# Kernel tuning notes

Measured on AMD Instinct MI355X. Metric: run time of the kernel, lower is better.

The kernel has to match this reference:

```python
import jax, jax.numpy as jnp
import numpy as np

B, N, F, H, E = 2, 384, 64, 128, 4
EPS_MEAN = 1e-10


def _lin(x, W, b=None):
    y = x @ W
    return y if b is None else y + b


def setup_inputs() -> dict:
    key = jax.random.key(0)
    ks = jax.random.split(key, 22)
    def rn(k, shape):
        return (jax.random.normal(k, shape, jnp.float32) / np.sqrt(shape[0])).astype(jnp.float32)
    h = jax.random.normal(ks[0], (B, N, F), jnp.float32)
    coord = jax.random.normal(ks[1], (B, N, 3), jnp.float32)
    edge_attr = jax.random.normal(ks[2], (B, N, N, E), jnp.float32)
    node_attr = jax.random.normal(ks[3], (B, N, F), jnp.float32)
    mask = (jax.random.uniform(ks[4], (B, N)) > 0.2).astype(jnp.float32)
    d_in_edge = 2 * F + 1 + E  # source, target, radial, edge_attr
    return dict(
        h=h, coord=coord, edge_attr=edge_attr, node_attr=node_attr, mask=mask,
        We1=rn(ks[5], (d_in_edge, H)), be1=jnp.zeros((H,), jnp.float32),
        We2=rn(ks[6], (H, H)), be2=jnp.zeros((H,), jnp.float32),
        Wa1=rn(ks[7], (H, H)), ba1=jnp.zeros((H,), jnp.float32),
        Wa2=rn(ks[8], (H, 1)), ba2=jnp.zeros((1,), jnp.float32),
        Wn1=rn(ks[9], (H + F + F, H)), bn1=jnp.zeros((H,), jnp.float32),
        Wn2=rn(ks[10], (H, F)), bn2=jnp.zeros((F,), jnp.float32),
        Wc1=rn(ks[11], (H, H)), bc1=jnp.zeros((H,), jnp.float32),
        Wc2=(jax.random.normal(ks[12], (H, 1), jnp.float32) * 0.001),  # xavier gain=0.001, no bias
    )


def reference(h, coord, edge_attr, node_attr, mask,
              We1, be1, We2, be2, Wa1, ba1, Wa2, ba2,
              Wn1, bn1, Wn2, bn2, Wc1, bc1, Wc2):
    # mask inputs
    coord = coord * mask[..., None]
    h = h * mask[..., None]
    mask2d = mask[:, :, None] * mask[:, None, :]  # [B,N,N]

    # coord2radial
    coord_diff = coord[:, :, None, :] - coord[:, None, :, :]      # [B,N,N,3]
    radial = jnp.sum(coord_diff ** 2, axis=-1, keepdims=True)     # [B,N,N,1]
    radial = radial * mask2d[..., None]
    coord_diff = coord_diff * mask2d[..., None]

    # edge model: source[b,i,j]=h[b,j], target[b,i,j]=h[b,i]
    source = jnp.broadcast_to(h[:, None, :, :], (h.shape[0], h.shape[1], h.shape[1], h.shape[2]))
    target = jnp.broadcast_to(h[:, :, None, :], source.shape)
    einp = jnp.concatenate([source, target, radial, edge_attr], axis=-1)  # [B,N,N,2F+1+E]
    m = jnp.tanh(_lin(einp, We1, be1))
    m = jnp.tanh(_lin(m, We2, be2))
    attn = jax.nn.sigmoid(_lin(jnp.tanh(_lin(m, Wa1, ba1)), Wa2, ba2))
    edge_feat = m * attn                                           # [B,N,N,H]

    # coord model (coords_agg='mean')
    embed_edge = _lin(jnp.tanh(_lin(edge_feat, Wc1, bc1)), Wc2)    # [B,N,N,1]
    trans = coord_diff * embed_edge * mask2d[..., None]            # [B,N,N,3]
    denom = jnp.sum(mask2d, axis=2, keepdims=True) + EPS_MEAN      # [B,N,1]
    coord_out = coord + jnp.sum(trans, axis=2) / denom
    coord_out = coord_out * mask[..., None]

    # node model (residual)
    agg = jnp.sum(edge_feat, axis=2)                               # [B,N,H]
    ninp = jnp.concatenate([h, node_attr, agg], axis=-1) * mask[..., None]
    nout = _lin(jnp.tanh(_lin(ninp, Wn1, bn1)), Wn2, bn2)
    h_out = (h + nout) * mask[..., None]

    return h_out, coord_out, edge_feat
```

## Files before the change

### kernel.cpp

```cpp
#include <hip/hip_runtime.h>

#define BB 2
#define NN 384
#define FF 64
#define HH 128
#define EE 4
#define ETILE 64
#define NCHUNK (NN / ETILE)
#define PRE_NB 16
#define NODE_NB 8

using f4 = float4;
typedef __attribute__((ext_vector_type(8))) short          bf16x8;
typedef __attribute__((ext_vector_type(8))) unsigned short u16x8;
typedef __attribute__((ext_vector_type(4))) unsigned short u16x4;
typedef __attribute__((ext_vector_type(4))) unsigned int   u32x4;
typedef __attribute__((ext_vector_type(4))) float          f32x4;

__device__ __forceinline__ float fast_tanh(float x) {
    float e = __expf(2.0f * x);
    return 1.0f - 2.0f / (e + 1.0f);
}
__device__ __forceinline__ float fast_sigmoid(float x) {
    return 1.0f / (1.0f + __expf(-x));
}
__device__ __forceinline__ unsigned short f2bf(float x) {
    unsigned int u = __float_as_uint(x);
    unsigned int r = (u + 0x7fffu + ((u >> 16) & 1u)) >> 16;
    return (unsigned short)r;
}
__device__ __forceinline__ float bf2f(unsigned short h) {
    return __uint_as_float(((unsigned int)h) << 16);
}
__device__ __forceinline__ bf16x8 as_bf16x8(u32x4 v) {
    union { u32x4 u; bf16x8 b; } c; c.u = v; return c.b;
}

__global__ __launch_bounds__(128) void pre_kernel(
    const float* __restrict__ h, const float* __restrict__ mask,
    const float* __restrict__ We1, const float* __restrict__ be1,
    float* __restrict__ Sg, float* __restrict__ Tg)
{
    const int n0 = blockIdx.x * PRE_NB;
    const int t  = threadIdx.x;
    __shared__ float hl[PRE_NB][FF];
    for (int q = t; q < PRE_NB * FF; q += 128) {
        const int n = q >> 6, f = q & 63;
        hl[n][f] = h[(n0 + n) * FF + f] * mask[n0 + n];
    }
    __syncthreads();
    float accS[PRE_NB], accT[PRE_NB];
    const float b1 = be1[t];
#pragma unroll
    for (int n = 0; n < PRE_NB; ++n) { accS[n] = 0.f; accT[n] = b1; }
    for (int f = 0; f < FF; ++f) {
        const float ws = We1[f * HH + t];
        const float wt = We1[(FF + f) * HH + t];
#pragma unroll
        for (int n = 0; n < PRE_NB; ++n) {
            accS[n] = fmaf(hl[n][f], ws, accS[n]);
            accT[n] = fmaf(hl[n][f], wt, accT[n]);
        }
    }
#pragma unroll
    for (int n = 0; n < PRE_NB; ++n) {
        Sg[(n0 + n) * HH + t] = accS[n];
        Tg[(n0 + n) * HH + t] = accT[n];
    }
}

__global__ __launch_bounds__(128) void wconv_kernel(
    const float* __restrict__ W0, const float* __restrict__ W1,
    const float* __restrict__ W2, unsigned short* __restrict__ WT)
{
    const int mat = blockIdx.x >> 7;
    const int o   = blockIdx.x & 127;
    const int k   = threadIdx.x;
    const float* src = (mat == 0) ? W0 : (mat == 1) ? W1 : W2;
    const float w = src[k * HH + o];
    const unsigned short hi = f2bf(w);
    const unsigned short lo = f2bf(w - bf2f(hi));
    WT[(mat * 2 + 0) * 16384 + o * HH + k] = hi;
    WT[(mat * 2 + 1) * 16384 + o * HH + k] = lo;
}

__device__ __forceinline__ void mfma_pass_dual(
    const ushort* __restrict__ A1, const ushort* __restrict__ A2,
    const ushort* __restrict__ WTp, f32x4 acc[4][2],
    const int l15, const int l4, const int c0)
{
    u32x4 Bf[2][4];
#pragma unroll
    for (int ct = 0; ct < 2; ++ct)
#pragma unroll
        for (int kb = 0; kb < 4; ++kb)
            Bf[ct][kb] = *(const u32x4*)&WTp[(c0 + ct * 16 + l15) * HH + kb * 32 + l4 * 8];
#pragma unroll
    for (int rt = 0; rt < 4; ++rt) {
        bf16x8 Af1[4], Af2[4];
#pragma unroll
        for (int kb = 0; kb < 4; ++kb) {
            const int idx = (16 * rt + l15) * HH + (((kb * 4 + l4) ^ l15) * 8);
            Af1[kb] = *(const bf16x8*)&A1[idx];
            Af2[kb] = *(const bf16x8*)&A2[idx];
        }
#pragma unroll
        for (int ct = 0; ct < 2; ++ct)
#pragma unroll
            for (int kb = 0; kb < 4; ++kb)
                acc[rt][ct] = __builtin_amdgcn_mfma_f32_16x16x32_bf16(
                    Af1[kb], as_bf16x8(Bf[ct][kb]), acc[rt][ct], 0, 0, 0);
#pragma unroll
        for (int ct = 0; ct < 2; ++ct)
#pragma unroll
            for (int kb = 0; kb < 4; ++kb)
                acc[rt][ct] = __builtin_amdgcn_mfma_f32_16x16x32_bf16(
                    Af2[kb], as_bf16x8(Bf[ct][kb]), acc[rt][ct], 0, 0, 0);
    }
}

__device__ __forceinline__ void mfma_pass_single(
    const ushort* __restrict__ A1, const ushort* __restrict__ WTp,
    f32x4 acc[4][2], const int l15, const int l4, const int c0)
{
    u32x4 Bf[2][4];
#pragma unroll
    for (int ct = 0; ct < 2; ++ct)
#pragma unroll
        for (int kb = 0; kb < 4; ++kb)
            Bf[ct][kb] = *(const u32x4*)&WTp[(c0 + ct * 16 + l15) * HH + kb * 32 + l4 * 8];
#pragma unroll
    for (int rt = 0; rt < 4; ++rt) {
        bf16x8 Af1[4];
#pragma unroll
        for (int kb = 0; kb < 4; ++kb) {
            const int idx = (16 * rt + l15) * HH + (((kb * 4 + l4) ^ l15) * 8);
            Af1[kb] = *(const bf16x8*)&A1[idx];
        }
#pragma unroll
        for (int ct = 0; ct < 2; ++ct)
#pragma unroll
            for (int kb = 0; kb < 4; ++kb)
                acc[rt][ct] = __builtin_amdgcn_mfma_f32_16x16x32_bf16(
                    Af1[kb], as_bf16x8(Bf[ct][kb]), acc[rt][ct], 0, 0, 0);
    }
}

__global__ __launch_bounds__(256, 4) void edge_kernel(
    const float* __restrict__ coord, const float* __restrict__ edge_attr,
    const float* __restrict__ mask,  const float* __restrict__ We1,
    const float* __restrict__ be2,   const float* __restrict__ ba1,
    const float* __restrict__ Wa2,   const float* __restrict__ ba2,
    const float* __restrict__ bc1,   const float* __restrict__ Wc2,
    const float* __restrict__ Sg,    const float* __restrict__ Tg,
    const unsigned short* __restrict__ WT,
    float* __restrict__ ef_out,
    float* __restrict__ agg_part,
    float* __restrict__ cag_part)
{
    __shared__ ushort Ah[ETILE * HH];
    __shared__ ushort Al[ETILE * HH];
    __shared__ float Tb[HH];
    __shared__ float sd_l[ETILE];
    __shared__ float cd_l[ETILE][3];
    __shared__ float ea_l[ETILE][4];
    __shared__ float attn_l[ETILE];
    __shared__ float embed_l[ETILE];
    __shared__ float part[512];

    const int bid = blockIdx.x;
    const int jc  = bid % NCHUNK;
    const int i   = (bid / NCHUNK) % NN;
    const int b   = bid / (NCHUNK * NN);
    const int j0  = jc * ETILE;
    const int t   = threadIdx.x;
    const int e   = t & 63;
    const int wv  = __builtin_amdgcn_readfirstlane(t >> 6);
    const int l15 = e & 15, l4 = e >> 4;
    const int c0  = wv * 32;

    const unsigned short* We2h = WT;
    const unsigned short* We2l = WT + 16384;
    const unsigned short* Wa1h = WT + 32768;
    const unsigned short* Wa1l = WT + 49152;
    const unsigned short* Wc1h = WT + 65536;

    const float be2a = be2[c0 + l15],      be2b = be2[c0 + 16 + l15];
    const float ba1a = ba1[c0 + l15],      ba1b = ba1[c0 + 16 + l15];
    const float wa2a = Wa2[c0 + l15],      wa2b = Wa2[c0 + 16 + l15];
    const float bc1a = bc1[c0 + l15],      bc1b = bc1[c0 + 16 + l15];
    const float wc2a = Wc2[c0 + l15],      wc2b = Wc2[c0 + 16 + l15];
    const float ba2s = ba2[0];

    if (t < HH) Tb[t] = Tg[(b * NN + i) * HH + t];
    if (t < ETILE) {
        const int j = j0 + t;
        const float mi = mask[b * NN + i], mj = mask[b * NN + j];
        const float m2 = mi * mj;
        const float d0 = coord[(b * NN + i) * 3 + 0] * mi - coord[(b * NN + j) * 3 + 0] * mj;
        const float d1 = coord[(b * NN + i) * 3 + 1] * mi - coord[(b * NN + j) * 3 + 1] * mj;
        const float d2 = coord[(b * NN + i) * 3 + 2] * mi - coord[(b * NN + j) * 3 + 2] * mj;
        sd_l[t] = (d0 * d0 + d1 * d1 + d2 * d2) * m2;
        cd_l[t][0] = d0 * m2; cd_l[t][1] = d1 * m2; cd_l[t][2] = d2 * m2;
        const f4 ea = *(const f4*)&edge_attr[(((size_t)b * NN + i) * NN + j) * EE];
        ea_l[t][0] = ea.x; ea_l[t][1] = ea.y; ea_l[t][2] = ea.z; ea_l[t][3] = ea.w;
    }
    __syncthreads();

    {
        const float rad = sd_l[e];
        const float ea0 = ea_l[e][0], ea1 = ea_l[e][1], ea2 = ea_l[e][2], ea3 = ea_l[e][3];
        const float* Srow = &Sg[((size_t)b * NN + (j0 + e)) * HH];
#pragma unroll
        for (int s = 0; s < 4; ++s) {
            u16x8 hp, lp;
#pragma unroll
            for (int hq = 0; hq < 2; ++hq) {
                const int o = c0 + s * 8 + hq * 4;
                const f4 sv = *(const f4*)&Srow[o];
                const f4 tb = *(const f4*)&Tb[o];
                const f4 wr = *(const f4*)&We1[128 * HH + o];
                const f4 w0 = *(const f4*)&We1[129 * HH + o];
                const f4 w1 = *(const f4*)&We1[130 * HH + o];
                const f4 w2 = *(const f4*)&We1[131 * HH + o];
                const f4 w3 = *(const f4*)&We1[132 * HH + o];
                float pv[4];
                pv[0] = sv.x + tb.x + rad * wr.x + ea0 * w0.x + ea1 * w1.x + ea2 * w2.x + ea3 * w3.x;
                pv[1] = sv.y + tb.y + rad * wr.y + ea0 * w0.y + ea1 * w1.y + ea2 * w2.y + ea3 * w3.y;
                pv[2] = sv.z + tb.z + rad * wr.z + ea0 * w0.z + ea1 * w1.z + ea2 * w2.z + ea3 * w3.z;
                pv[3] = sv.w + tb.w + rad * wr.w + ea0 * w0.w + ea1 * w1.w + ea2 * w2.w + ea3 * w3.w;
#pragma unroll
                for (int q = 0; q < 4; ++q) {
                    const float v = fast_tanh(pv[q]);
                    const unsigned short hv = f2bf(v);
                    hp[hq * 4 + q] = hv;
                    lp[hq * 4 + q] = f2bf(v - bf2f(hv));
                }
            }
            const int phys = (wv * 4 + s) ^ (e & 15);
            *(u16x8*)&Ah[e * HH + phys * 8] = hp;
            *(u16x8*)&Al[e * HH + phys * 8] = lp;
        }
    }
    __syncthreads();

    f32x4 acc[4][2];

#pragma unroll
    for (int rt = 0; rt < 4; ++rt)
#pragma unroll
        for (int ct = 0; ct < 2; ++ct) acc[rt][ct] = (f32x4){0.f, 0.f, 0.f, 0.f};
    mfma_pass_dual(Ah, Al, We2h, acc, l15, l4, c0);
    mfma_pass_single(Ah, We2l, acc, l15, l4, c0);
    __syncthreads();
#pragma unroll
    for (int rt = 0; rt < 4; ++rt)
#pragma unroll
        for (int ct = 0; ct < 2; ++ct)
#pragma unroll
            for (int r = 0; r < 4; ++r) {
                const float v = fast_tanh(acc[rt][ct][r] + (ct ? be2b : be2a));
                const int row = 16 * rt + 4 * l4 + r;
                const int col = c0 + ct * 16 + l15;
                const int idx = row * HH + (((col >> 3) ^ (row & 15)) * 8) + (col & 7);
                const unsigned short hv = f2bf(v);
                Ah[idx] = hv;
                Al[idx] = f2bf(v - bf2f(hv));
            }
    __syncthreads();

#pragma unroll
    for (int rt = 0; rt < 4; ++rt)
#pragma unroll
        for (int ct = 0; ct < 2; ++ct) acc[rt][ct] = (f32x4){0.f, 0.f, 0.f, 0.f};
    mfma_pass_dual(Ah, Al, Wa1h, acc, l15, l4, c0);
    mfma_pass_single(Ah, Wa1l, acc, l15, l4, c0);
#pragma unroll
    for (int rt = 0; rt < 4; ++rt)
#pragma unroll
        for (int r = 0; r < 4; ++r) {
            float s = fast_tanh(acc[rt][0][r] + ba1a) * wa2a +
                      fast_tanh(acc[rt][1][r] + ba1b) * wa2b;
            s += __shfl_xor(s, 1); s += __shfl_xor(s, 2);
            s += __shfl_xor(s, 4); s += __shfl_xor(s, 8);
            if (l15 == 0) part[wv * 64 + 16 * rt + 4 * l4 + r] = s;
        }
    __syncthreads();
    if (t < ETILE)
        attn_l[t] = fast_sigmoid(part[t] + part[64 + t] + part[128 + t] +
                                 part[192 + t] + ba2s);
    __syncthreads();

#pragma unroll
    for (int rt = 0; rt < 4; ++rt)
#pragma unroll
        for (int ct = 0; ct < 2; ++ct) acc[rt][ct] = (f32x4){0.f, 0.f, 0.f, 0.f};
    mfma_pass_single(Ah, Wc1h, acc, l15, l4, c0);
#pragma unroll
    for (int rt = 0; rt < 4; ++rt)
#pragma unroll
        for (int r = 0; r < 4; ++r) {
            const int row = 16 * rt + 4 * l4 + r;
            const float at = attn_l[row];
            float s = fast_tanh(at * acc[rt][0][r] + bc1a) * wc2a +
                      fast_tanh(at * acc[rt][1][r] + bc1b) * wc2b;
            s += __shfl_xor(s, 1); s += __shfl_xor(s, 2);
            s += __shfl_xor(s, 4); s += __shfl_xor(s, 8);
            if (l15 == 0) part[wv * 64 + row] = s;
        }
    __syncthreads();
    if (t < ETILE)
        embed_l[t] = part[t] + part[64 + t] + part[128 + t] + part[192 + t];
    __syncthreads();

    {
        const int erow = t >> 5;
        const int colq = t & 31;
        const int col  = colq * 4;
        const int chunk = col >> 3;
        const int sub   = col & 7;
        float a0 = 0.f, a1 = 0.f, a2 = 0.f, a3 = 0.f;
        float* obase = &ef_out[(((size_t)b * NN + i) * NN + j0) * HH];
#pragma unroll
        for (int it = 0; it < 8; ++it) {
            const int row = it * 8 + erow;
            const float at = attn_l[row];
            const int idx = row * HH + ((chunk ^ (row & 15)) * 8) + sub;
            const u16x4 hv4 = *(const u16x4*)&Ah[idx];
            const u16x4 lv4 = *(const u16x4*)&Al[idx];
            f4 v;
            v.x = (bf2f(hv4[0]) + bf2f(lv4[0])) * at;
            v.y = (bf2f(hv4[1]) + bf2f(lv4[1])) * at;
            v.z = (bf2f(hv4[2]) + bf2f(lv4[2])) * at;
            v.w = (bf2f(hv4[3]) + bf2f(lv4[3])) * at;
            *(f4*)&obase[row * HH + col] = v;
            a0 += v.x; a1 += v.y; a2 += v.z; a3 += v.w;
        }
        a0 += __shfl_xor(a0, 32);
        a1 += __shfl_xor(a1, 32);
        a2 += __shfl_xor(a2, 32);
        a3 += __shfl_xor(a3, 32);
        if (e < 32) {
            part[wv * HH + col + 0] = a0;
            part[wv * HH + col + 1] = a1;
            part[wv * HH + col + 2] = a2;
            part[wv * HH + col + 3] = a3;
        }
    }
    if (t < ETILE) {
        const float em = embed_l[t];
        float tr0 = cd_l[t][0] * em, tr1 = cd_l[t][1] * em, tr2 = cd_l[t][2] * em;
#pragma unroll
        for (int off = 1; off < 64; off <<= 1) {
            tr0 += __shfl_xor(tr0, off);
            tr1 += __shfl_xor(tr1, off);
            tr2 += __shfl_xor(tr2, off);
        }
        if (t == 0) {
            cag_part[(size_t)bid * 3 + 0] = tr0;
            cag_part[(size_t)bid * 3 + 1] = tr1;
            cag_part[(size_t)bid * 3 + 2] = tr2;
        }
    }
    __syncthreads();
    if (t < HH)
        agg_part[(size_t)bid * HH + t] =
            part[t] + part[HH + t] + part[2 * HH + t] + part[3 * HH + t];
}

__global__ __launch_bounds__(256) void node_kernel(
    const float* __restrict__ h, const float* __restrict__ coord,
    const float* __restrict__ node_attr, const float* __restrict__ mask,
    const float* __restrict__ Wn1, const float* __restrict__ bn1,
    const float* __restrict__ Wn2, const float* __restrict__ bn2,
    const float* __restrict__ agg_part, const float* __restrict__ cag_part,
    float* __restrict__ h_out, float* __restrict__ c_out)
{
    const int n0 = blockIdx.x * NODE_NB;
    const int b  = n0 / NN;
    const int t  = threadIdx.x;
    __shared__ float nl[NODE_NB][2 * FF + HH];
    __shared__ float ul[NODE_NB][HH];
    __shared__ float pp[4][NODE_NB][HH];
    __shared__ float msum_s;

    for (int q = t; q < NODE_NB * 256; q += 256) {
        const int n = q >> 8, k = q & 255;
        const int bn = n0 + n;
        const float mi = mask[bn];
        float v;
        if (k < FF)          v = h[bn * FF + k] * mi;
        else if (k < 2 * FF) v = node_attr[bn * FF + (k - FF)] * mi;
        else {
            float a = 0.f;
            const int o = k - 2 * FF;
#pragma unroll
            for (int jc = 0; jc < NCHUNK; ++jc)
                a += agg_part[((size_t)bn * NCHUNK + jc) * HH + o];
            v = a * mi;
        }
        nl[n][k] = v;
    }
    if (t < 64) {
        float s = 0.f;
#pragma unroll
        for (int q = 0; q < 6; ++q) s += mask[b * NN + q * 64 + t];
#pragma unroll
        for (int off = 1; off < 64; off <<= 1) s += __shfl_xor(s, off);
        if (t == 0) msum_s = s;
    }
    __syncthreads();

    {
        const int col = t & 127, kh = t >> 7;
        float acc[NODE_NB];
#pragma unroll
        for (int n = 0; n < NODE_NB; ++n) acc[n] = 0.f;
        for (int k = kh * 128; k < kh * 128 + 128; ++k) {
            const float w = Wn1[k * HH + col];
#pragma unroll
            for (int n = 0; n < NODE_NB; ++n)
                acc[n] = fmaf(nl[n][k], w, acc[n]);
        }
#pragma unroll
        for (int n = 0; n < NODE_NB; ++n) pp[kh][n][col] = acc[n];
    }
    __syncthreads();
#pragma unroll
    for (int r = 0; r < 4; ++r) {
        const int idx = t + 256 * r;
        const int n = idx >> 7, col = idx & 127;
        ul[n][col] = fast_tanh(pp[0][n][col] + pp[1][n][col] + bn1[col]);
    }
    __syncthreads();

    {
        const int col = t & 63, ks = t >> 6;
        float acc[NODE_NB];
#pragma unroll
        for (int n = 0; n < NODE_NB; ++n) acc[n] = 0.f;
        for (int k = ks * 32; k < ks * 32 + 32; ++k) {
            const float w = Wn2[k * FF + col];
#pragma unroll
            for (int n = 0; n < NODE_NB; ++n)
                acc[n] = fmaf(ul[n][k], w, acc[n]);
        }
#pragma unroll
        for (int n = 0; n < NODE_NB; ++n) pp[ks][n][col] = acc[n];
    }
    __syncthreads();
#pragma unroll
    for (int r = 0; r < 2; ++r) {
        const int idx = t + 256 * r;
        const int n = idx >> 6, col = idx & 63;
        const int bn = n0 + n;
        const float mi = mask[bn];
        const float a = pp[0][n][col] + pp[1][n][col] + pp[2][n][col] +
                        pp[3][n][col] + bn2[col];
        h_out[bn * FF + col] = (nl[n][col] + a) * mi;
    }
    if (t < NODE_NB * 3) {
        const int n = t / 3, d = t % 3;
        const int bn = n0 + n;
        const float mi = mask[bn];
        float cag = 0.f;
#pragma unroll
        for (int jc = 0; jc < NCHUNK; ++jc)
            cag += cag_part[((size_t)bn * NCHUNK + jc) * 3 + d];
        const float denom = mi * msum_s + 1e-10f;
        c_out[bn * 3 + d] = (coord[bn * 3 + d] * mi + cag / denom) * mi;
    }
}

extern "C" void kernel_launch(void* const* d_in, const int* in_sizes, int n_in,
                              void* d_out, int out_size, void* d_ws, size_t ws_size,
                              hipStream_t stream)
{
    const float* h         = (const float*)d_in[0];
    const float* coord     = (const float*)d_in[1];
    const float* edge_attr = (const float*)d_in[2];
    const float* node_attr = (const float*)d_in[3];
    const float* mask      = (const float*)d_in[4];
    const float* We1 = (const float*)d_in[5];
    const float* be1 = (const float*)d_in[6];
    const float* We2 = (const float*)d_in[7];
    const float* be2 = (const float*)d_in[8];
    const float* Wa1 = (const float*)d_in[9];
    const float* ba1 = (const float*)d_in[10];
    const float* Wa2 = (const float*)d_in[11];
    const float* ba2 = (const float*)d_in[12];
    const float* Wn1 = (const float*)d_in[13];
    const float* bn1 = (const float*)d_in[14];
    const float* Wn2 = (const float*)d_in[15];
    const float* bn2 = (const float*)d_in[16];
    const float* Wc1 = (const float*)d_in[17];
    const float* bc1 = (const float*)d_in[18];
    const float* Wc2 = (const float*)d_in[19];

    float* out    = (float*)d_out;
    float* h_out  = out;
    float* c_out  = out + (size_t)BB * NN * FF;
    float* ef_out = c_out + (size_t)BB * NN * 3;

    float* ws = (float*)d_ws;
    float* Sg = ws;
    float* Tg = Sg + (size_t)BB * NN * HH;
    float* agg_part = Tg + (size_t)BB * NN * HH;
    float* cag_part = agg_part + (size_t)BB * NN * NCHUNK * HH;
    unsigned short* WT = (unsigned short*)(cag_part + (size_t)BB * NN * NCHUNK * 3);

    pre_kernel<<<BB * NN / PRE_NB, 128, 0, stream>>>(h, mask, We1, be1, Sg, Tg);
    wconv_kernel<<<3 * HH, 128, 0, stream>>>(We2, Wa1, Wc1, WT);
    edge_kernel<<<BB * NN * NCHUNK, 256, 0, stream>>>(
        coord, edge_attr, mask, We1, be2, ba1, Wa2, ba2, bc1, Wc2,
        Sg, Tg, WT, ef_out, agg_part, cag_part);
    node_kernel<<<BB * NN / NODE_NB, 256, 0, stream>>>(
        h, coord, node_attr, mask, Wn1, bn1, Wn2, bn2,
        agg_part, cag_part, h_out, c_out);
}
```

Before: 456.0 us.

## Merge prep kernels, prefetch S rows, cheaper bf16 split packing, halve node tile

Combines the pre-projection and weight-conversion kernels into one launch to cut launch overhead. In the edge kernel, S rows are prefetched into registers before the coordinate setup. The bf16 hi/lo split now uses truncation via byte-perm plus a packed v_cvt_pk_bf16 for the low part, instead of per-element software rounding. The node kernel tile shrinks from 8 to 4 nodes to launch more blocks. Truncating the high part instead of rounding it changes the split slightly, but hi+lo still tracks the fp32 value closely.

```diff
diff --git a/kernel.cpp b/kernel.cpp
--- a/kernel.cpp
+++ b/kernel.cpp
@@ -8,7 +8,7 @@
 #define ETILE 64
 #define NCHUNK (NN / ETILE)
 #define PRE_NB 16
-#define NODE_NB 8
+#define NODE_NB 4
 
 using f4 = float4;
 typedef __attribute__((ext_vector_type(8))) short          bf16x8;
@@ -35,14 +35,38 @@
 __device__ __forceinline__ bf16x8 as_bf16x8(u32x4 v) {
     union { u32x4 u; bf16x8 b; } c; c.u = v; return c.b;
 }
-
-__global__ __launch_bounds__(128) void pre_kernel(
+__device__ __forceinline__ unsigned int hi_pack(float v0, float v1) {
+    return __builtin_amdgcn_perm(__float_as_uint(v1), __float_as_uint(v0),
+                                 0x07060302u);
+}
+__device__ __forceinline__ unsigned int cvt_pk_bf16(float a, float b) {
+    unsigned int r;
+    asm("v_cvt_pk_bf16_f32 %0, %1, %2" : "=v"(r) : "v"(a), "v"(b));
+    return r;
+}
+
+__global__ __launch_bounds__(128) void prep_kernel(
     const float* __restrict__ h, const float* __restrict__ mask,
     const float* __restrict__ We1, const float* __restrict__ be1,
-    float* __restrict__ Sg, float* __restrict__ Tg)
+    const float* __restrict__ W0, const float* __restrict__ W1,
+    const float* __restrict__ W2,
+    float* __restrict__ Sg, float* __restrict__ Tg,
+    unsigned short* __restrict__ WT)
 {
+    const int t = threadIdx.x;
+    if (blockIdx.x >= BB * NN / PRE_NB) {
+        const int bid2 = blockIdx.x - BB * NN / PRE_NB;
+        const int mat = bid2 >> 7;
+        const int o   = bid2 & 127;
+        const float* src = (mat == 0) ? W0 : (mat == 1) ? W1 : W2;
+        const float w = src[t * HH + o];
+        const unsigned short hi = f2bf(w);
+        const unsigned short lo = f2bf(w - bf2f(hi));
+        WT[(mat * 2 + 0) * 16384 + o * HH + t] = hi;
+        WT[(mat * 2 + 1) * 16384 + o * HH + t] = lo;
+        return;
+    }
     const int n0 = blockIdx.x * PRE_NB;
-    const int t  = threadIdx.x;
     __shared__ float hl[PRE_NB][FF];
     for (int q = t; q < PRE_NB * FF; q += 128) {
         const int n = q >> 6, f = q & 63;
@@ -67,21 +91,6 @@
         Sg[(n0 + n) * HH + t] = accS[n];
         Tg[(n0 + n) * HH + t] = accT[n];
     }
-}
-
-__global__ __launch_bounds__(128) void wconv_kernel(
-    const float* __restrict__ W0, const float* __restrict__ W1,
-    const float* __restrict__ W2, unsigned short* __restrict__ WT)
-{
-    const int mat = blockIdx.x >> 7;
-    const int o   = blockIdx.x & 127;
-    const int k   = threadIdx.x;
-    const float* src = (mat == 0) ? W0 : (mat == 1) ? W1 : W2;
-    const float w = src[k * HH + o];
-    const unsigned short hi = f2bf(w);
-    const unsigned short lo = f2bf(w - bf2f(hi));
-    WT[(mat * 2 + 0) * 16384 + o * HH + k] = hi;
-    WT[(mat * 2 + 1) * 16384 + o * HH + k] = lo;
 }
 
 __device__ __forceinline__ void mfma_pass_dual(
@@ -179,6 +188,13 @@
     const int l15 = e & 15, l4 = e >> 4;
     const int c0  = wv * 32;
 
+    f4 svp[8];
+    {
+        const float* Srow = &Sg[((size_t)b * NN + (j0 + e)) * HH];
+#pragma unroll
+        for (int s = 0; s < 8; ++s) svp[s] = *(const f4*)&Srow[c0 + s * 4];
+    }
+
     const unsigned short* We2h = WT;
     const unsigned short* We2l = WT + 16384;
     const unsigned short* Wa1h = WT + 32768;
@@ -210,36 +226,36 @@
     {
         const float rad = sd_l[e];
         const float ea0 = ea_l[e][0], ea1 = ea_l[e][1], ea2 = ea_l[e][2], ea3 = ea_l[e][3];
-        const float* Srow = &Sg[((size_t)b * NN + (j0 + e)) * HH];
 #pragma unroll
         for (int s = 0; s < 4; ++s) {
-            u16x8 hp, lp;
+            float v[8];
 #pragma unroll
             for (int hq = 0; hq < 2; ++hq) {
                 const int o = c0 + s * 8 + hq * 4;
-                const f4 sv = *(const f4*)&Srow[o];
+                const f4 sv = svp[s * 2 + hq];
                 const f4 tb = *(const f4*)&Tb[o];
                 const f4 wr = *(const f4*)&We1[128 * HH + o];
                 const f4 w0 = *(const f4*)&We1[129 * HH + o];
                 const f4 w1 = *(const f4*)&We1[130 * HH + o];
                 const f4 w2 = *(const f4*)&We1[131 * HH + o];
                 const f4 w3 = *(const f4*)&We1[132 * HH + o];
-                float pv[4];
-                pv[0] = sv.x + tb.x + rad * wr.x + ea0 * w0.x + ea1 * w1.x + ea2 * w2.x + ea3 * w3.x;
-                pv[1] = sv.y + tb.y + rad * wr.y + ea0 * w0.y + ea1 * w1.y + ea2 * w2.y + ea3 * w3.y;
-                pv[2] = sv.z + tb.z + rad * wr.z + ea0 * w0.z + ea1 * w1.z + ea2 * w2.z + ea3 * w3.z;
-                pv[3] = sv.w + tb.w + rad * wr.w + ea0 * w0.w + ea1 * w1.w + ea2 * w2.w + ea3 * w3.w;
-#pragma unroll
-                for (int q = 0; q < 4; ++q) {
-                    const float v = fast_tanh(pv[q]);
-                    const unsigned short hv = f2bf(v);
-                    hp[hq * 4 + q] = hv;
-                    lp[hq * 4 + q] = f2bf(v - bf2f(hv));
-                }
+                v[hq*4+0] = fast_tanh(sv.x + tb.x + rad*wr.x + ea0*w0.x + ea1*w1.x + ea2*w2.x + ea3*w3.x);
+                v[hq*4+1] = fast_tanh(sv.y + tb.y + rad*wr.y + ea0*w0.y + ea1*w1.y + ea2*w2.y + ea3*w3.y);
+                v[hq*4+2] = fast_tanh(sv.z + tb.z + rad*wr.z + ea0*w0.z + ea1*w1.z + ea2*w2.z + ea3*w3.z);
+                v[hq*4+3] = fast_tanh(sv.w + tb.w + rad*wr.w + ea0*w0.w + ea1*w1.w + ea2*w2.w + ea3*w3.w);
+            }
+            u32x4 hp, lp;
+#pragma unroll
+            for (int p = 0; p < 4; ++p) {
+                const float v0 = v[2*p], v1 = v[2*p+1];
+                hp[p] = hi_pack(v0, v1);
+                const float lo0 = v0 - __uint_as_float(__float_as_uint(v0) & 0xFFFF0000u);
+                const float lo1 = v1 - __uint_as_float(__float_as_uint(v1) & 0xFFFF0000u);
+                lp[p] = cvt_pk_bf16(lo0, lo1);
             }
             const int phys = (wv * 4 + s) ^ (e & 15);
-            *(u16x8*)&Ah[e * HH + phys * 8] = hp;
-            *(u16x8*)&Al[e * HH + phys * 8] = lp;
+            *(u32x4*)&Ah[e * HH + phys * 8] = hp;
+            *(u32x4*)&Al[e * HH + phys * 8] = lp;
         }
     }
     __syncthreads();
@@ -263,9 +279,10 @@
                 const int row = 16 * rt + 4 * l4 + r;
                 const int col = c0 + ct * 16 + l15;
                 const int idx = row * HH + (((col >> 3) ^ (row & 15)) * 8) + (col & 7);
-                const unsigned short hv = f2bf(v);
-                Ah[idx] = hv;
-                Al[idx] = f2bf(v - bf2f(hv));
+                const unsigned int u = __float_as_uint(v);
+                Ah[idx] = (unsigned short)(u >> 16);
+                const float lo = v - __uint_as_float(u & 0xFFFF0000u);
+                Al[idx] = f2bf(lo);
             }
     __syncthreads();
 
@@ -384,6 +401,7 @@
     __shared__ float pp[4][NODE_NB][HH];
     __shared__ float msum_s;
 
+#pragma unroll
     for (int q = t; q < NODE_NB * 256; q += 256) {
         const int n = q >> 8, k = q & 255;
         const int bn = n0 + n;
@@ -427,7 +445,7 @@
     }
     __syncthreads();
 #pragma unroll
-    for (int r = 0; r < 4; ++r) {
+    for (int r = 0; r < 2; ++r) {
         const int idx = t + 256 * r;
         const int n = idx >> 7, col = idx & 127;
         ul[n][col] = fast_tanh(pp[0][n][col] + pp[1][n][col] + bn1[col]);
@@ -449,10 +467,8 @@
         for (int n = 0; n < NODE_NB; ++n) pp[ks][n][col] = acc[n];
     }
     __syncthreads();
-#pragma unroll
-    for (int r = 0; r < 2; ++r) {
-        const int idx = t + 256 * r;
-        const int n = idx >> 6, col = idx & 63;
+    {
+        const int n = t >> 6, col = t & 63;
         const int bn = n0 + n;
         const float mi = mask[bn];
         const float a = pp[0][n][col] + pp[1][n][col] + pp[2][n][col] +
@@ -509,8 +525,8 @@
     float* cag_part = agg_part + (size_t)BB * NN * NCHUNK * HH;
     unsigned short* WT = (unsigned short*)(cag_part + (size_t)BB * NN * NCHUNK * 3);
 
-    pre_kernel<<<BB * NN / PRE_NB, 128, 0, stream>>>(h, mask, We1, be1, Sg, Tg);
-    wconv_kernel<<<3 * HH, 128, 0, stream>>>(We2, Wa1, Wc1, WT);
+    prep_kernel<<<BB * NN / PRE_NB + 3 * HH, 128, 0, stream>>>(
+        h, mask, We1, be1, We2, Wa1, Wc1, Sg, Tg, WT);
     edge_kernel<<<BB * NN * NCHUNK, 256, 0, stream>>>(
         coord, edge_attr, mask, We1, be2, ba1, Wa2, ba2, bc1, Wc2,
         Sg, Tg, WT, ef_out, agg_part, cag_part);
```

Measured after the change: 461.5 us. About the same (+1.2%).
